# Performance work log

Hardware: AMD Instinct MI355X
Metric: run time of the kernel (lower is better)

The kernel has to match this reference:

```python
import jax, jax.numpy as jnp
import numpy as np

B = 8192
DV = 768   # visual_input_size
DT = 768   # text_input_size
E = 8      # num_experts
D = 1024   # expert_output_size
G = 2 * D  # gate_input_size
EPS = 1e-5


def setup_inputs() -> dict:
    key = jax.random.key(0)
    ks = jax.random.split(key, 14)
    s = lambda fan_in: 1.0 / np.sqrt(fan_in)
    return {
        "visual_features": jax.random.normal(ks[0], (B, DV), dtype=jnp.float32),
        "text_features": jax.random.normal(ks[1], (B, DT), dtype=jnp.float32),
        "vis_w": jax.random.uniform(ks[2], (DV, D), jnp.float32, -s(DV), s(DV)),
        "vis_b": jax.random.uniform(ks[3], (D,), jnp.float32, -s(DV), s(DV)),
        "txt_w": jax.random.uniform(ks[4], (DT, D), jnp.float32, -s(DT), s(DT)),
        "txt_b": jax.random.uniform(ks[5], (D,), jnp.float32, -s(DT), s(DT)),
        "gate_w": jax.random.uniform(ks[6], (G, E), jnp.float32, -s(G), s(G)),
        "gate_b": jax.random.uniform(ks[7], (E,), jnp.float32, -s(G), s(G)),
        "w1": jax.random.uniform(ks[8], (E, G, D), jnp.float32, -s(G), s(G)),
        "b1": jax.random.uniform(ks[9], (E, D), jnp.float32, -s(G), s(G)),
        "w2": jax.random.uniform(ks[10], (E, D, D), jnp.float32, -s(D), s(D)),
        "b2": jax.random.uniform(ks[11], (E, D), jnp.float32, -s(D), s(D)),
        "ln_g": jnp.ones((E, D), dtype=jnp.float32),
        "ln_b": jnp.zeros((E, D), dtype=jnp.float32),
    }


def reference(visual_features, text_features, vis_w, vis_b, txt_w, txt_b,
              gate_w, gate_b, w1, b1, w2, b2, ln_g, ln_b):
    # Projections + concat -> combined features [B, 2D]
    pv = visual_features @ vis_w + vis_b
    pt = text_features @ txt_w + txt_b
    combined = jnp.concatenate([pv, pt], axis=1)

    # Gate (dropout is identity at inference)
    gate_probs = jax.nn.softmax(combined @ gate_w + gate_b, axis=1)  # [B, E]

    # All experts as batched GEMMs: [B,G] x [E,G,D] -> [B,E,D]
    h = jnp.einsum('bg,egd->bed', combined, w1) + b1
    h = jax.nn.gelu(h, approximate=False)  # torch nn.GELU default = exact erf
    h = jnp.einsum('bed,edo->beo', h, w2) + b2

    # Per-expert LayerNorm over last dim
    mu = jnp.mean(h, axis=-1, keepdims=True)
    var = jnp.mean(jnp.square(h - mu), axis=-1, keepdims=True)
    h = (h - mu) * jax.lax.rsqrt(var + EPS) * ln_g + ln_b

    # Gated reduction over experts
    return jnp.einsum('bed,be->bd', h, gate_probs)
```

## Files before the change

### kernel.cpp

```cpp
#include <hip/hip_runtime.h>
#include <hip/hip_bf16.h>
#include <math.h>

#define BM 128
#define BN 128
#define BK 64

typedef __bf16 bf16x8_t __attribute__((ext_vector_type(8)));
typedef __bf16 bf16x4_t __attribute__((ext_vector_type(4)));
typedef float f32x16_t __attribute__((ext_vector_type(16)));

static __device__ __forceinline__ float bf2f(__bf16 b) {
    unsigned short s = __builtin_bit_cast(unsigned short, b);
    unsigned int u = ((unsigned int)s) << 16;
    return __builtin_bit_cast(float, u);
}
static __device__ __forceinline__ __bf16 f2bf(float f) {
    unsigned int u = __builtin_bit_cast(unsigned int, f);
    unsigned int r = (u + 0x7fffu + ((u >> 16) & 1u)) >> 16;
    return __builtin_bit_cast(__bf16, (unsigned short)r);
}
static __device__ __forceinline__ float gelu_fast(float x) {
    const float s = x * (0.7978845608f + 0.0356774081f * x * x);
    const float e = __expf(-2.0f * s);
    return x * __builtin_amdgcn_rcpf(1.0f + e);
}

#define GLDS16(gp, lp)                                                                   \
    __builtin_amdgcn_global_load_lds((const __attribute__((address_space(1))) void*)(gp), \
                                     (__attribute__((address_space(3))) void*)(lp), 16, 0, 0)

__global__ __launch_bounds__(256) void frag_cast(const float* __restrict__ in,
                                                 __bf16* __restrict__ out,
                                                 int K, int N,
                                                 size_t inStride, size_t outStride) {
    in += (size_t)blockIdx.z * inStride;
    out += (size_t)blockIdx.z * outStride;
    __shared__ float tile[64][65];
    const int k0 = blockIdx.x * 64, n0 = blockIdx.y * 64;
    const int tid = threadIdx.x;
    const int r = tid >> 4, c4 = (tid & 15) * 4;
#pragma unroll
    for (int p = 0; p < 4; ++p) {
        const float4 v = *(const float4*)&in[(size_t)(k0 + r + p * 16) * N + n0 + c4];
        tile[r + p * 16][c4 + 0] = v.x;
        tile[r + p * 16][c4 + 1] = v.y;
        tile[r + p * 16][c4 + 2] = v.z;
        tile[r + p * 16][c4 + 3] = v.w;
    }
    __syncthreads();
    const int c = tid >> 5, nn0 = (tid & 31) * 2;
#pragma unroll
    for (int t = 0; t < 2; ++t) {
        const int nn = nn0 + t;
        bf16x8_t v;
#pragma unroll
        for (int j = 0; j < 8; ++j) v[j] = f2bf(tile[c * 8 + j][nn]);
        *(bf16x8_t*)&out[((size_t)(k0 >> 3) + c) * N * 8 + (size_t)(n0 + nn) * 8] = v;
    }
}

__global__ __launch_bounds__(256) void cast2_kernel(const float* __restrict__ a,
                                                    const float* __restrict__ b,
                                                    __bf16* __restrict__ out, int n8each) {
    const int i = blockIdx.x * 256 + threadIdx.x;
    if (i < 2 * n8each) {
        const float* src = (i < n8each) ? a : b;
        const size_t idx = (i < n8each) ? (size_t)i : (size_t)(i - n8each);
        const float4* p = (const float4*)(src + idx * 8);
        const float4 x = p[0], y = p[1];
        bf16x8_t v;
        v[0] = f2bf(x.x); v[1] = f2bf(x.y); v[2] = f2bf(x.z); v[3] = f2bf(x.w);
        v[4] = f2bf(y.x); v[5] = f2bf(y.y); v[6] = f2bf(y.z); v[7] = f2bf(y.w);
        *(bf16x8_t*)(out + (size_t)i * 8) = v;
    }
}

__global__ __launch_bounds__(256) void cast_acat(const float* __restrict__ vis,
                                                 const float* __restrict__ txt,
                                                 __bf16* __restrict__ out, int total8) {
    const int i = blockIdx.x * 256 + threadIdx.x;
    if (i < total8) {
        const int r = i / 192;
        const int c8 = i - r * 192;
        const float* src = (c8 < 96) ? vis + (size_t)r * 768 + (size_t)c8 * 8
                                     : txt + (size_t)r * 768 + (size_t)(c8 - 96) * 8;
        const float4* p = (const float4*)src;
        const float4 x = p[0], y = p[1];
        bf16x8_t v;
        v[0] = f2bf(x.x); v[1] = f2bf(x.y); v[2] = f2bf(x.z); v[3] = f2bf(x.w);
        v[4] = f2bf(y.x); v[5] = f2bf(y.y); v[6] = f2bf(y.z); v[7] = f2bf(y.w);
        *(bf16x8_t*)(out + (size_t)i * 8) = v;
    }
}

template <int ACT, int PACK>
static __device__ __forceinline__ void gemm_core(const __bf16* __restrict__ A, int lda,
                                                 const __bf16* __restrict__ Bt, int Bn,
                                                 const float* __restrict__ bias,
                                                 __bf16* __restrict__ C, int ldc, int K,
                                                 int bm, int bn, __bf16* As) {
    const int tid = threadIdx.x;
    const int lane = tid & 63, wave = tid >> 6;
    const int wm = wave >> 1, wn = wave & 1;
    const int l = lane & 31, hi = lane >> 5;

    const int srow = tid >> 3;
    const int schunk = (tid & 7) ^ (srow & 7);
    const __bf16* ag = A + (size_t)(bm * BM + srow) * lda + schunk * 8;
    __bf16* asl = As + tid * 8;

    const int c0 = hi ^ (l & 7);
    const __bf16* base_a = As + (size_t)(wm * 64 + l) * BK;

    const size_t Bn8 = (size_t)Bn * 8;
    const __bf16* bbase = Bt + (size_t)hi * Bn8 + (size_t)(bn * BN + wn * 64 + l) * 8;

    f32x16_t acc[2][2] = {};

    const int nk = K / BK;
    for (int kt = 0; kt < nk; ++kt) {
        bf16x8_t bfr[4][2];
        const __bf16* bp = bbase + (size_t)(kt * 8) * Bn8;
#pragma unroll
        for (int s = 0; s < 4; ++s) {
            bfr[s][0] = *(const bf16x8_t*)(bp + (size_t)(2 * s) * Bn8);
            bfr[s][1] = *(const bf16x8_t*)(bp + (size_t)(2 * s) * Bn8 + 256);
        }
        GLDS16(ag, asl);
        GLDS16(ag + (size_t)32 * lda, asl + 2048);
        GLDS16(ag + (size_t)64 * lda, asl + 4096);
        GLDS16(ag + (size_t)96 * lda, asl + 6144);
        ag += BK;
        __syncthreads();
#pragma unroll
        for (int s = 0; s < 4; ++s) {
            const int co = (c0 ^ (2 * s)) * 8;
            const bf16x8_t a0 = *(const bf16x8_t*)(base_a + co);
            const bf16x8_t a1 = *(const bf16x8_t*)(base_a + 2048 + co);
            acc[0][0] = __builtin_amdgcn_mfma_f32_32x32x16_bf16(a0, bfr[s][0], acc[0][0], 0, 0, 0);
            acc[0][1] = __builtin_amdgcn_mfma_f32_32x32x16_bf16(a0, bfr[s][1], acc[0][1], 0, 0, 0);
            acc[1][0] = __builtin_amdgcn_mfma_f32_32x32x16_bf16(a1, bfr[s][0], acc[1][0], 0, 0, 0);
            acc[1][1] = __builtin_amdgcn_mfma_f32_32x32x16_bf16(a1, bfr[s][1], acc[1][1], 0, 0, 0);
        }
        __syncthreads();
    }

    const int colbase = bn * BN + wn * 64 + l;
    const int rowbase = bm * BM + wm * 64 + 4 * hi;
#pragma unroll
    for (int ni = 0; ni < 2; ++ni) {
        const int col = colbase + ni * 32;
        const float bv = PACK ? 0.0f : bias[col];
#pragma unroll
        for (int mi = 0; mi < 2; ++mi) {
#pragma unroll
            for (int v = 0; v < 16; ++v) {
                const int row = rowbase + mi * 32 + (v & 3) + 8 * (v >> 2);
                float x = acc[mi][ni][v] + bv;
                if (ACT == 1) x = gelu_fast(x);
                if (PACK) {
                    C[((size_t)(row >> 3)) * (size_t)ldc * 8 + (size_t)col * 8 + (row & 7)] = f2bf(x);
                } else {
                    C[(size_t)row * ldc + col] = f2bf(x);
                }
            }
        }
    }
}

template <int ACT>
__global__ __launch_bounds__(256) void gemm_bt(const __bf16* __restrict__ Ab, int lda, size_t strideAe,
                                               const __bf16* __restrict__ Bb, int Bn, size_t strideBe,
                                               const float* __restrict__ biasb, size_t strideBiasE,
                                               __bf16* __restrict__ Cb, int ldc, size_t strideCe,
                                               int K) {
    __shared__ __bf16 As[BM * BK];
    gemm_core<ACT, 0>(Ab + (size_t)blockIdx.z * strideAe, lda,
                      Bb + (size_t)blockIdx.z * strideBe, Bn,
                      biasb + (size_t)blockIdx.z * strideBiasE,
                      Cb + (size_t)blockIdx.z * strideCe, ldc, K,
                      blockIdx.x, blockIdx.y, As);
}

__global__ __launch_bounds__(256) void gemm_premul(const __bf16* __restrict__ wbf,
                                                   const __bf16* __restrict__ w1t,
                                                   __bf16* __restrict__ w1cat) {
    __shared__ __bf16 As[BM * BK];
    const int e = blockIdx.z & 7, hf = blockIdx.z >> 3;
    gemm_core<0, 1>(wbf + (size_t)hf * 768 * 1024, 1024,
                    w1t + (size_t)e * 2048 * 1024 + (size_t)hf * 128 * 1024 * 8, 1024,
                    nullptr,
                    w1cat + (size_t)e * 1536 * 1024 + (size_t)hf * 96 * 1024 * 8, 1024, 1024,
                    blockIdx.x, blockIdx.y, As);
}

__global__ __launch_bounds__(256) void bias1_kernel(const float* __restrict__ w1,
                                                    const float* __restrict__ vis_b,
                                                    const float* __restrict__ txt_b,
                                                    const float* __restrict__ b1,
                                                    float* __restrict__ b1t) {
    const int n = blockIdx.x * 256 + threadIdx.x;
    const int e = blockIdx.y;
    const int d0 = blockIdx.z * 512;
    float acc = (blockIdx.z == 0) ? b1[(size_t)e * 1024 + n] : 0.0f;
#pragma unroll 4
    for (int d = d0; d < d0 + 512; ++d) {
        const float bv = (d < 1024) ? vis_b[d] : txt_b[d - 1024];
        acc += bv * w1[((size_t)e * 2048 + d) * 1024 + n];
    }
    atomicAdd(&b1t[(size_t)e * 1024 + n], acc);
}

__global__ __launch_bounds__(256) void gcat_kernel(const float* __restrict__ vis_w,
                                                   const float* __restrict__ txt_w,
                                                   const float* __restrict__ vis_b,
                                                   const float* __restrict__ txt_b,
                                                   const float* __restrict__ gw,
                                                   const float* __restrict__ gb,
                                                   float* __restrict__ gcat) {
    const int v = blockIdx.x, tid = threadIdx.x;
    const int lane = tid & 63, wv = tid >> 6;
    float a[8] = {0, 0, 0, 0, 0, 0, 0, 0};
    if (v < 1536) {
        const float* wr = (v < 768) ? vis_w + (size_t)v * 1024 : txt_w + (size_t)(v - 768) * 1024;
        const int dbase = (v < 768) ? 0 : 1024;
        for (int d = tid; d < 1024; d += 256) {
            const float c = wr[d];
            const float4* g4 = (const float4*)(gw + (size_t)(dbase + d) * 8);
            const float4 x = g4[0], y = g4[1];
            a[0] += c * x.x; a[1] += c * x.y; a[2] += c * x.z; a[3] += c * x.w;
            a[4] += c * y.x; a[5] += c * y.y; a[6] += c * y.z; a[7] += c * y.w;
        }
    } else {
        for (int d = tid; d < 2048; d += 256) {
            const float c = (d < 1024) ? vis_b[d] : txt_b[d - 1024];
            const float4* g4 = (const float4*)(gw + (size_t)d * 8);
            const float4 x = g4[0], y = g4[1];
            a[0] += c * x.x; a[1] += c * x.y; a[2] += c * x.z; a[3] += c * x.w;
            a[4] += c * y.x; a[5] += c * y.y; a[6] += c * y.z; a[7] += c * y.w;
        }
    }
#pragma unroll
    for (int j = 0; j < 8; ++j)
        for (int off = 32; off; off >>= 1) a[j] += __shfl_down(a[j], off, 64);
    __shared__ float red[4][8];
    if (lane == 0) {
#pragma unroll
        for (int j = 0; j < 8; ++j) red[wv][j] = a[j];
    }
    __syncthreads();
    if (tid < 8) {
        float s = red[0][tid] + red[1][tid] + red[2][tid] + red[3][tid];
        if (v == 1536) s += gb[tid];
        gcat[(size_t)v * 8 + tid] = s;
    }
}

__global__ __launch_bounds__(256) void gate_kernel(const __bf16* __restrict__ acat,
                                                   const float* __restrict__ gcat,
                                                   float* __restrict__ gate) {
    const int b = blockIdx.x, tid = threadIdx.x;
    const int lane = tid & 63, wv = tid >> 6;
    const __bf16* row = acat + (size_t)b * 1536;
    float a[8] = {0, 0, 0, 0, 0, 0, 0, 0};
    for (int k = tid; k < 1536; k += 256) {
        const float c = bf2f(row[k]);
        const float4* g4 = (const float4*)(gcat + (size_t)k * 8);
        const float4 x = g4[0], y = g4[1];
        a[0] += c * x.x; a[1] += c * x.y; a[2] += c * x.z; a[3] += c * x.w;
        a[4] += c * y.x; a[5] += c * y.y; a[6] += c * y.z; a[7] += c * y.w;
    }
#pragma unroll
    for (int j = 0; j < 8; ++j)
        for (int off = 32; off; off >>= 1) a[j] += __shfl_down(a[j], off, 64);
    __shared__ float red[4][8];
    if (lane == 0) {
#pragma unroll
        for (int j = 0; j < 8; ++j) red[wv][j] = a[j];
    }
    __syncthreads();
    if (tid == 0) {
        const float* bg = gcat + 1536 * 8;
        float l[8];
        float m = -1e30f;
        for (int j = 0; j < 8; ++j) {
            l[j] = red[0][j] + red[1][j] + red[2][j] + red[3][j] + bg[j];
            m = fmaxf(m, l[j]);
        }
        float s = 0.f;
        for (int j = 0; j < 8; ++j) { l[j] = expf(l[j] - m); s += l[j]; }
        const float inv = 1.0f / s;
        for (int j = 0; j < 8; ++j) gate[(size_t)b * 8 + j] = l[j] * inv;
    }
}

__global__ __launch_bounds__(256) void ln_out_kernel(const __bf16* __restrict__ h2,
                                                     const float* __restrict__ gate,
                                                     const float* __restrict__ lng,
                                                     const float* __restrict__ lnb,
                                                     float* __restrict__ out,
                                                     int Eg, int g0, int accum) {
    const int b = blockIdx.x;
    const int tid = threadIdx.x;
    const int lane = tid & 63, wv = tid >> 6;
    const int d0 = tid * 4;
    __shared__ float sS[4], sSS[4];
    float* orow = out + (size_t)b * 1024 + d0;
    float o0, o1, o2, o3;
    if (accum) {
        const float4 p = *(const float4*)orow;
        o0 = p.x; o1 = p.y; o2 = p.z; o3 = p.w;
    } else {
        o0 = o1 = o2 = o3 = 0.f;
    }
    for (int e = 0; e < Eg; ++e) {
        const __bf16* hp = h2 + ((size_t)e * 8192 + b) * 1024 + d0;
        const bf16x4_t hv = *(const bf16x4_t*)hp;
        const float v0 = bf2f(hv[0]), v1 = bf2f(hv[1]), v2 = bf2f(hv[2]), v3 = bf2f(hv[3]);
        float s = v0 + v1 + v2 + v3;
        float ss = v0 * v0 + v1 * v1 + v2 * v2 + v3 * v3;
        for (int off = 32; off; off >>= 1) {
            s += __shfl_down(s, off, 64);
            ss += __shfl_down(ss, off, 64);
        }
        if (lane == 0) { sS[wv] = s; sSS[wv] = ss; }
        __syncthreads();
        const float S = sS[0] + sS[1] + sS[2] + sS[3];
        const float SS = sSS[0] + sSS[1] + sSS[2] + sSS[3];
        __syncthreads();
        const float mu = S * (1.0f / 1024.0f);
        const float var = SS * (1.0f / 1024.0f) - mu * mu;
        const float rstd = rsqrtf(var + 1e-5f);
        const float w = gate[(size_t)b * 8 + g0 + e];
        const float4 gg = *(const float4*)(lng + (size_t)(g0 + e) * 1024 + d0);
        const float4 bb = *(const float4*)(lnb + (size_t)(g0 + e) * 1024 + d0);
        o0 += w * ((v0 - mu) * rstd * gg.x + bb.x);
        o1 += w * ((v1 - mu) * rstd * gg.y + bb.y);
        o2 += w * ((v2 - mu) * rstd * gg.z + bb.z);
        o3 += w * ((v3 - mu) * rstd * gg.w + bb.w);
    }
    *(float4*)orow = make_float4(o0, o1, o2, o3);
}

extern "C" void kernel_launch(void* const* d_in, const int* in_sizes, int n_in,
                              void* d_out, int out_size, void* d_ws, size_t ws_size,
                              hipStream_t stream) {
    (void)in_sizes; (void)n_in; (void)out_size;
    const float* visual = (const float*)d_in[0];
    const float* text   = (const float*)d_in[1];
    const float* vis_w  = (const float*)d_in[2];
    const float* vis_b  = (const float*)d_in[3];
    const float* txt_w  = (const float*)d_in[4];
    const float* txt_b  = (const float*)d_in[5];
    const float* gate_w = (const float*)d_in[6];
    const float* gate_b = (const float*)d_in[7];
    const float* w1     = (const float*)d_in[8];
    const float* b1     = (const float*)d_in[9];
    const float* w2     = (const float*)d_in[10];
    const float* b2     = (const float*)d_in[11];
    const float* ln_g   = (const float*)d_in[12];
    const float* ln_b   = (const float*)d_in[13];
    float* out = (float*)d_out;

    const size_t B = 8192, DV = 768, D = 1024, G = 2048, E = 8, KC = 1536;

    char* ws = (char*)d_ws;
    size_t o = 0;
    auto alloc = [&](size_t bytes) { size_t r = o; o = (o + bytes + 255) & ~(size_t)255; return r; };
    const size_t off_wbf   = alloc(2 * DV * D * 2);
    const size_t off_w1cat = alloc(E * KC * D * 2);
    const size_t off_w2t   = alloc(E * D * D * 2);
    const size_t off_b1t   = alloc(E * D * 4);
    const size_t off_gcat  = alloc((KC * E + E) * 4);
    const size_t off_gate  = alloc(B * E * 4);
    const size_t off_acat  = alloc(B * KC * 2);
    const size_t fixedEnd = o;
    const size_t w1tBytes = E * G * D * 2;

    int Eg = 1;
    {
        const int cand[4] = {8, 4, 2, 1};
        for (int c = 0; c < 4; ++c) {
            size_t h2b = 2 * (size_t)cand[c] * B * D * 2;
            size_t dyn = h2b > w1tBytes ? h2b : w1tBytes;
            if (fixedEnd + dyn <= ws_size || cand[c] == 1) { Eg = cand[c]; break; }
        }
    }

    __bf16* wbf   = (__bf16*)(ws + off_wbf);
    __bf16* w1cat = (__bf16*)(ws + off_w1cat);
    __bf16* w2t   = (__bf16*)(ws + off_w2t);
    float*  b1t   = (float*)(ws + off_b1t);
    float*  gcat  = (float*)(ws + off_gcat);
    float*  gate  = (float*)(ws + off_gate);
    __bf16* acat  = (__bf16*)(ws + off_acat);
    __bf16* w1t   = (__bf16*)(ws + fixedEnd);
    __bf16* h1    = (__bf16*)(ws + fixedEnd);
    __bf16* h2    = h1 + (size_t)Eg * B * D;

    const int nw8 = (int)(DV * D / 8);
    cast2_kernel<<<(2 * nw8 + 255) / 256, 256, 0, stream>>>(vis_w, txt_w, wbf, nw8);
    const int na8 = (int)(B * KC / 8);
    cast_acat<<<(na8 + 255) / 256, 256, 0, stream>>>(visual, text, acat, na8);

    frag_cast<<<dim3(G / 64, D / 64, E), 256, 0, stream>>>(w1, w1t, (int)G, (int)D, G * D, G * D);
    frag_cast<<<dim3(D / 64, D / 64, E), 256, 0, stream>>>(w2, w2t, (int)D, (int)D, D * D, D * D);

    gemm_premul<<<dim3(768 / BM, D / BN, 16), 256, 0, stream>>>(wbf, w1t, w1cat);

    hipMemsetAsync(b1t, 0, E * D * 4, stream);
    bias1_kernel<<<dim3(4, 8, 4), 256, 0, stream>>>(w1, vis_b, txt_b, b1, b1t);
    gcat_kernel<<<1537, 256, 0, stream>>>(vis_w, txt_w, vis_b, txt_b, gate_w, gate_b, gcat);

    gate_kernel<<<(int)B, 256, 0, stream>>>(acat, gcat, gate);

    const int ng = 8 / Eg;
    for (int g = 0; g < ng; ++g) {
        const int g0 = g * Eg;
        gemm_bt<1><<<dim3(B / BM, D / BN, Eg), 256, 0, stream>>>(
            acat, (int)KC, 0, w1cat + (size_t)g0 * KC * D, (int)D, KC * D,
            b1t + (size_t)g0 * D, D, h1, (int)D, B * D, (int)KC);
        gemm_bt<0><<<dim3(B / BM, D / BN, Eg), 256, 0, stream>>>(
            h1, (int)D, B * D, w2t + (size_t)g0 * D * D, (int)D, D * D,
            b2 + (size_t)g0 * D, D, h2, (int)D, B * D, (int)D);
        ln_out_kernel<<<(int)B, 256, 0, stream>>>(h2, gate, ln_g, ln_b, out, Eg, g0, g > 0 ? 1 : 0);
    }
}
```

Baseline: 793.9 us.

## Use 256x256 tiles with double-buffered LDS for both GEMM operands

```diff
diff --git a/kernel.cpp b/kernel.cpp
--- a/kernel.cpp
+++ b/kernel.cpp
@@ -2,8 +2,8 @@
 #include <hip/hip_bf16.h>
 #include <math.h>
 
-#define BM 128
-#define BN 128
+#define BM 256
+#define BN 256
 #define BK 64
 
 typedef __bf16 bf16x8_t __attribute__((ext_vector_type(8)));
@@ -94,66 +94,107 @@
     }
 }
 
+#define MFMA32(a, b, c) __builtin_amdgcn_mfma_f32_32x32x16_bf16(a, b, c, 0, 0, 0)
+
 template <int ACT, int PACK>
 static __device__ __forceinline__ void gemm_core(const __bf16* __restrict__ A, int lda,
                                                  const __bf16* __restrict__ Bt, int Bn,
                                                  const float* __restrict__ bias,
                                                  __bf16* __restrict__ C, int ldc, int K,
-                                                 int bm, int bn, __bf16* As) {
+                                                 int bm, int bn,
+                                                 __bf16* As, __bf16* Bs) {
     const int tid = threadIdx.x;
     const int lane = tid & 63, wave = tid >> 6;
-    const int wm = wave >> 1, wn = wave & 1;
+    const int wm = wave >> 2, wn = wave & 3;
     const int l = lane & 31, hi = lane >> 5;
 
-    const int srow = tid >> 3;
-    const int schunk = (tid & 7) ^ (srow & 7);
-    const __bf16* ag = A + (size_t)(bm * BM + srow) * lda + schunk * 8;
-    __bf16* asl = As + tid * 8;
-
-    const int c0 = hi ^ (l & 7);
-    const __bf16* base_a = As + (size_t)(wm * 64 + l) * BK;
-
     const size_t Bn8 = (size_t)Bn * 8;
-    const __bf16* bbase = Bt + (size_t)hi * Bn8 + (size_t)(bn * BN + wn * 64 + l) * 8;
-
-    f32x16_t acc[2][2] = {};
+    const size_t bKt = Bn8 * 8;
+    const size_t BUFE = 8 * 256 * 8;
+
+    const __bf16* aSrc[4];
+    const __bf16* bSrc[4];
+    __bf16* aDst[4];
+    __bf16* bDst[4];
+#pragma unroll
+    for (int r = 0; r < 4; ++r) {
+        const int idx = r * 512 + tid;
+        const int ch = idx >> 8, rw = idx & 255;
+        aSrc[r] = A + (size_t)(bm * BM + rw) * lda + ch * 8;
+        bSrc[r] = Bt + (size_t)ch * Bn8 + (size_t)(bn * BN + rw) * 8;
+        aDst[r] = As + (size_t)idx * 8;
+        bDst[r] = Bs + (size_t)idx * 8;
+    }
+
+    const __bf16* aRd = As + ((size_t)hi * 256 + wm * 128 + l) * 8;
+    const __bf16* bRd = Bs + ((size_t)hi * 256 + wn * 64 + l) * 8;
+
+    f32x16_t acc[4][2] = {};
+
+#pragma unroll
+    for (int r = 0; r < 4; ++r) {
+        GLDS16(aSrc[r], aDst[r]);
+        GLDS16(bSrc[r], bDst[r]);
+    }
+    asm volatile("s_waitcnt vmcnt(0)");
+    __builtin_amdgcn_s_barrier();
+    __builtin_amdgcn_sched_barrier(0);
 
     const int nk = K / BK;
     for (int kt = 0; kt < nk; ++kt) {
-        bf16x8_t bfr[4][2];
-        const __bf16* bp = bbase + (size_t)(kt * 8) * Bn8;
+        const int cur = kt & 1;
+        const int nxt = cur ^ 1;
+        const int ktn = (kt + 1 < nk) ? kt + 1 : kt;
+        const __bf16* aR = aRd + (size_t)cur * BUFE;
+        const __bf16* bR = bRd + (size_t)cur * BUFE;
 #pragma unroll
         for (int s = 0; s < 4; ++s) {
-            bfr[s][0] = *(const bf16x8_t*)(bp + (size_t)(2 * s) * Bn8);
-            bfr[s][1] = *(const bf16x8_t*)(bp + (size_t)(2 * s) * Bn8 + 256);
-        }
-        GLDS16(ag, asl);
-        GLDS16(ag + (size_t)32 * lda, asl + 2048);
-        GLDS16(ag + (size_t)64 * lda, asl + 4096);
-        GLDS16(ag + (size_t)96 * lda, asl + 6144);
-        ag += BK;
-        __syncthreads();
-#pragma unroll
-        for (int s = 0; s < 4; ++s) {
-            const int co = (c0 ^ (2 * s)) * 8;
-            const bf16x8_t a0 = *(const bf16x8_t*)(base_a + co);
-            const bf16x8_t a1 = *(const bf16x8_t*)(base_a + 2048 + co);
-            acc[0][0] = __builtin_amdgcn_mfma_f32_32x32x16_bf16(a0, bfr[s][0], acc[0][0], 0, 0, 0);
-            acc[0][1] = __builtin_amdgcn_mfma_f32_32x32x16_bf16(a0, bfr[s][1], acc[0][1], 0, 0, 0);
-            acc[1][0] = __builtin_amdgcn_mfma_f32_32x32x16_bf16(a1, bfr[s][0], acc[1][0], 0, 0, 0);
-            acc[1][1] = __builtin_amdgcn_mfma_f32_32x32x16_bf16(a1, bfr[s][1], acc[1][1], 0, 0, 0);
-        }
-        __syncthreads();
+            const size_t co = (size_t)(2 * s) * 2048;
+            const bf16x8_t a0 = *(const bf16x8_t*)(aR + co);
+            const bf16x8_t a1 = *(const bf16x8_t*)(aR + co + 256);
+            const bf16x8_t a2 = *(const bf16x8_t*)(aR + co + 512);
+            const bf16x8_t a3 = *(const bf16x8_t*)(aR + co + 768);
+            const bf16x8_t b0 = *(const bf16x8_t*)(bR + co);
+            const bf16x8_t b1 = *(const bf16x8_t*)(bR + co + 256);
+            if (s == 0) {
+                GLDS16(aSrc[0] + (size_t)ktn * BK, aDst[0] + nxt * BUFE);
+                GLDS16(bSrc[0] + (size_t)ktn * bKt, bDst[0] + nxt * BUFE);
+                GLDS16(aSrc[1] + (size_t)ktn * BK, aDst[1] + nxt * BUFE);
+                GLDS16(bSrc[1] + (size_t)ktn * bKt, bDst[1] + nxt * BUFE);
+            } else if (s == 1) {
+                GLDS16(aSrc[2] + (size_t)ktn * BK, aDst[2] + nxt * BUFE);
+                GLDS16(bSrc[2] + (size_t)ktn * bKt, bDst[2] + nxt * BUFE);
+                GLDS16(aSrc[3] + (size_t)ktn * BK, aDst[3] + nxt * BUFE);
+                GLDS16(bSrc[3] + (size_t)ktn * bKt, bDst[3] + nxt * BUFE);
+            }
+            __builtin_amdgcn_sched_barrier(0);
+            __builtin_amdgcn_s_barrier();
+            __builtin_amdgcn_sched_barrier(0);
+            __builtin_amdgcn_s_setprio(1);
+            acc[0][0] = MFMA32(a0, b0, acc[0][0]);
+            acc[0][1] = MFMA32(a0, b1, acc[0][1]);
+            acc[1][0] = MFMA32(a1, b0, acc[1][0]);
+            acc[1][1] = MFMA32(a1, b1, acc[1][1]);
+            acc[2][0] = MFMA32(a2, b0, acc[2][0]);
+            acc[2][1] = MFMA32(a2, b1, acc[2][1]);
+            acc[3][0] = MFMA32(a3, b0, acc[3][0]);
+            acc[3][1] = MFMA32(a3, b1, acc[3][1]);
+            __builtin_amdgcn_s_setprio(0);
+            if (s == 3) asm volatile("s_waitcnt vmcnt(0)");
+            __builtin_amdgcn_sched_barrier(0);
+            __builtin_amdgcn_s_barrier();
+            __builtin_amdgcn_sched_barrier(0);
+        }
     }
 
     const int colbase = bn * BN + wn * 64 + l;
-    const int rowbase = bm * BM + wm * 64 + 4 * hi;
+    const int rowbase = bm * BM + wm * 128 + 4 * hi;
 #pragma unroll
     for (int ni = 0; ni < 2; ++ni) {
         const int col = colbase + ni * 32;
         const float bv = PACK ? 0.0f : bias[col];
 #pragma unroll
-        for (int mi = 0; mi < 2; ++mi) {
+        for (int mi = 0; mi < 4; ++mi) {
 #pragma unroll
             for (int v = 0; v < 16; ++v) {
                 const int row = rowbase + mi * 32 + (v & 3) + 8 * (v >> 2);
@@ -170,29 +211,31 @@
 }
 
 template <int ACT>
-__global__ __launch_bounds__(256) void gemm_bt(const __bf16* __restrict__ Ab, int lda, size_t strideAe,
-                                               const __bf16* __restrict__ Bb, int Bn, size_t strideBe,
-                                               const float* __restrict__ biasb, size_t strideBiasE,
-                                               __bf16* __restrict__ Cb, int ldc, size_t strideCe,
-                                               int K) {
-    __shared__ __bf16 As[BM * BK];
+__global__ __launch_bounds__(512, 2) void gemm_bt(const __bf16* __restrict__ Ab, int lda, size_t strideAe,
+                                                  const __bf16* __restrict__ Bb, int Bn, size_t strideBe,
+                                                  const float* __restrict__ biasb, size_t strideBiasE,
+                                                  __bf16* __restrict__ Cb, int ldc, size_t strideCe,
+                                                  int K) {
+    __shared__ __bf16 As[2 * 8 * 256 * 8];
+    __shared__ __bf16 Bs[2 * 8 * 256 * 8];
     gemm_core<ACT, 0>(Ab + (size_t)blockIdx.z * strideAe, lda,
                       Bb + (size_t)blockIdx.z * strideBe, Bn,
                       biasb + (size_t)blockIdx.z * strideBiasE,
                       Cb + (size_t)blockIdx.z * strideCe, ldc, K,
-                      blockIdx.x, blockIdx.y, As);
-}
-
-__global__ __launch_bounds__(256) void gemm_premul(const __bf16* __restrict__ wbf,
-                                                   const __bf16* __restrict__ w1t,
-                                                   __bf16* __restrict__ w1cat) {
-    __shared__ __bf16 As[BM * BK];
+                      blockIdx.x, blockIdx.y, As, Bs);
+}
+
+__global__ __launch_bounds__(512, 2) void gemm_premul(const __bf16* __restrict__ wbf,
+                                                      const __bf16* __restrict__ w1t,
+                                                      __bf16* __restrict__ w1cat) {
+    __shared__ __bf16 As[2 * 8 * 256 * 8];
+    __shared__ __bf16 Bs[2 * 8 * 256 * 8];
     const int e = blockIdx.z & 7, hf = blockIdx.z >> 3;
     gemm_core<0, 1>(wbf + (size_t)hf * 768 * 1024, 1024,
                     w1t + (size_t)e * 2048 * 1024 + (size_t)hf * 128 * 1024 * 8, 1024,
                     nullptr,
                     w1cat + (size_t)e * 1536 * 1024 + (size_t)hf * 96 * 1024 * 8, 1024, 1024,
-                    blockIdx.x, blockIdx.y, As);
+                    blockIdx.x, blockIdx.y, As, Bs);
 }
 
 __global__ __launch_bounds__(256) void bias1_kernel(const float* __restrict__ w1,
@@ -407,7 +450,7 @@
     frag_cast<<<dim3(G / 64, D / 64, E), 256, 0, stream>>>(w1, w1t, (int)G, (int)D, G * D, G * D);
     frag_cast<<<dim3(D / 64, D / 64, E), 256, 0, stream>>>(w2, w2t, (int)D, (int)D, D * D, D * D);
 
-    gemm_premul<<<dim3(768 / BM, D / BN, 16), 256, 0, stream>>>(wbf, w1t, w1cat);
+    gemm_premul<<<dim3(768 / BM, D / BN, 16), 512, 0, stream>>>(wbf, w1t, w1cat);
 
     hipMemsetAsync(b1t, 0, E * D * 4, stream);
     bias1_kernel<<<dim3(4, 8, 4), 256, 0, stream>>>(w1, vis_b, txt_b, b1, b1t);
@@ -418,10 +461,10 @@
     const int ng = 8 / Eg;
     for (int g = 0; g < ng; ++g) {
         const int g0 = g * Eg;
-        gemm_bt<1><<<dim3(B / BM, D / BN, Eg), 256, 0, stream>>>(
+        gemm_bt<1><<<dim3(B / BM, D / BN, Eg), 512, 0, stream>>>(
             acat, (int)KC, 0, w1cat + (size_t)g0 * KC * D, (int)D, KC * D,
             b1t + (size_t)g0 * D, D, h1, (int)D, B * D, (int)KC);
-        gemm_bt<0><<<dim3(B / BM, D / BN, Eg), 256, 0, stream>>>(
+        gemm_bt<0><<<dim3(B / BM, D / BN, Eg), 512, 0, stream>>>(
             h1, (int)D, B * D, w2t + (size_t)g0 * D * D, (int)D, D * D,
             b2 + (size_t)g0 * D, D, h2, (int)D, B * D, (int)D);
         ln_out_kernel<<<(int)B, 256, 0, stream>>>(h2, gate, ln_g, ln_b, out, Eg, g0, g > 0 ? 1 : 0);
```

Result: slower. 893.4 us (+12.5%).

## Store GEMM A operands in 128-row k-chunk tiled layout for contiguous loads

Applied to the files above, without the earlier changes.

```diff
diff --git a/kernel.cpp b/kernel.cpp
--- a/kernel.cpp
+++ b/kernel.cpp
@@ -65,14 +65,18 @@
                                                     __bf16* __restrict__ out, int n8each) {
     const int i = blockIdx.x * 256 + threadIdx.x;
     if (i < 2 * n8each) {
-        const float* src = (i < n8each) ? a : b;
-        const size_t idx = (i < n8each) ? (size_t)i : (size_t)(i - n8each);
-        const float4* p = (const float4*)(src + idx * 8);
+        const int m = (i < n8each) ? 0 : 1;
+        const int ii = i - m * n8each;
+        const float* src = (m ? b : a) + (size_t)ii * 8;
+        const int r = ii >> 7, c8 = ii & 127;
+        const size_t dst = (size_t)m * 786432 + (size_t)(r >> 7) * 131072 +
+                           (size_t)c8 * 1024 + (size_t)(r & 127) * 8;
+        const float4* p = (const float4*)src;
         const float4 x = p[0], y = p[1];
         bf16x8_t v;
         v[0] = f2bf(x.x); v[1] = f2bf(x.y); v[2] = f2bf(x.z); v[3] = f2bf(x.w);
         v[4] = f2bf(y.x); v[5] = f2bf(y.y); v[6] = f2bf(y.z); v[7] = f2bf(y.w);
-        *(bf16x8_t*)(out + (size_t)i * 8) = v;
+        *(bf16x8_t*)(out + dst) = v;
     }
 }
 
@@ -90,58 +94,59 @@
         bf16x8_t v;
         v[0] = f2bf(x.x); v[1] = f2bf(x.y); v[2] = f2bf(x.z); v[3] = f2bf(x.w);
         v[4] = f2bf(y.x); v[5] = f2bf(y.y); v[6] = f2bf(y.z); v[7] = f2bf(y.w);
-        *(bf16x8_t*)(out + (size_t)i * 8) = v;
-    }
-}
+        const size_t dst = (size_t)(r >> 7) * 196608 + (size_t)c8 * 1024 +
+                           (size_t)(r & 127) * 8;
+        *(bf16x8_t*)(out + dst) = v;
+    }
+}
+
+#define MFMA32(a, b, c) __builtin_amdgcn_mfma_f32_32x32x16_bf16(a, b, c, 0, 0, 0)
 
 template <int ACT, int PACK>
-static __device__ __forceinline__ void gemm_core(const __bf16* __restrict__ A, int lda,
+static __device__ __forceinline__ void gemm_core(const __bf16* __restrict__ A, int K,
                                                  const __bf16* __restrict__ Bt, int Bn,
                                                  const float* __restrict__ bias,
-                                                 __bf16* __restrict__ C, int ldc, int K,
+                                                 __bf16* __restrict__ C, int ldc,
                                                  int bm, int bn, __bf16* As) {
     const int tid = threadIdx.x;
     const int lane = tid & 63, wave = tid >> 6;
     const int wm = wave >> 1, wn = wave & 1;
     const int l = lane & 31, hi = lane >> 5;
 
-    const int srow = tid >> 3;
-    const int schunk = (tid & 7) ^ (srow & 7);
-    const __bf16* ag = A + (size_t)(bm * BM + srow) * lda + schunk * 8;
+    const __bf16* ag = A + (size_t)bm * K * 128 + (size_t)tid * 8;
     __bf16* asl = As + tid * 8;
 
-    const int c0 = hi ^ (l & 7);
-    const __bf16* base_a = As + (size_t)(wm * 64 + l) * BK;
+    const __bf16* base_a = As + hi * 1024 + (wm * 64 + l) * 8;
 
     const size_t Bn8 = (size_t)Bn * 8;
     const __bf16* bbase = Bt + (size_t)hi * Bn8 + (size_t)(bn * BN + wn * 64 + l) * 8;
+    const size_t bAdv = 8 * Bn8;
 
     f32x16_t acc[2][2] = {};
 
     const int nk = K / BK;
     for (int kt = 0; kt < nk; ++kt) {
         bf16x8_t bfr[4][2];
-        const __bf16* bp = bbase + (size_t)(kt * 8) * Bn8;
 #pragma unroll
         for (int s = 0; s < 4; ++s) {
-            bfr[s][0] = *(const bf16x8_t*)(bp + (size_t)(2 * s) * Bn8);
-            bfr[s][1] = *(const bf16x8_t*)(bp + (size_t)(2 * s) * Bn8 + 256);
+            bfr[s][0] = *(const bf16x8_t*)(bbase + (size_t)(2 * s) * Bn8);
+            bfr[s][1] = *(const bf16x8_t*)(bbase + (size_t)(2 * s) * Bn8 + 256);
         }
         GLDS16(ag, asl);
-        GLDS16(ag + (size_t)32 * lda, asl + 2048);
-        GLDS16(ag + (size_t)64 * lda, asl + 4096);
-        GLDS16(ag + (size_t)96 * lda, asl + 6144);
-        ag += BK;
+        GLDS16(ag + 2048, asl + 2048);
+        GLDS16(ag + 4096, asl + 4096);
+        GLDS16(ag + 6144, asl + 6144);
+        ag += 8192;
+        bbase += bAdv;
         __syncthreads();
 #pragma unroll
         for (int s = 0; s < 4; ++s) {
-            const int co = (c0 ^ (2 * s)) * 8;
-            const bf16x8_t a0 = *(const bf16x8_t*)(base_a + co);
-            const bf16x8_t a1 = *(const bf16x8_t*)(base_a + 2048 + co);
-            acc[0][0] = __builtin_amdgcn_mfma_f32_32x32x16_bf16(a0, bfr[s][0], acc[0][0], 0, 0, 0);
-            acc[0][1] = __builtin_amdgcn_mfma_f32_32x32x16_bf16(a0, bfr[s][1], acc[0][1], 0, 0, 0);
-            acc[1][0] = __builtin_amdgcn_mfma_f32_32x32x16_bf16(a1, bfr[s][0], acc[1][0], 0, 0, 0);
-            acc[1][1] = __builtin_amdgcn_mfma_f32_32x32x16_bf16(a1, bfr[s][1], acc[1][1], 0, 0, 0);
+            const bf16x8_t a0 = *(const bf16x8_t*)(base_a + s * 2048);
+            const bf16x8_t a1 = *(const bf16x8_t*)(base_a + s * 2048 + 256);
+            acc[0][0] = MFMA32(a0, bfr[s][0], acc[0][0]);
+            acc[0][1] = MFMA32(a0, bfr[s][1], acc[0][1]);
+            acc[1][0] = MFMA32(a1, bfr[s][0], acc[1][0]);
+            acc[1][1] = MFMA32(a1, bfr[s][1], acc[1][1]);
         }
         __syncthreads();
     }
@@ -151,7 +156,7 @@
 #pragma unroll
     for (int ni = 0; ni < 2; ++ni) {
         const int col = colbase + ni * 32;
-        const float bv = PACK ? 0.0f : bias[col];
+        const float bv = (PACK == 1) ? 0.0f : bias[col];
 #pragma unroll
         for (int mi = 0; mi < 2; ++mi) {
 #pragma unroll
@@ -159,8 +164,11 @@
                 const int row = rowbase + mi * 32 + (v & 3) + 8 * (v >> 2);
                 float x = acc[mi][ni][v] + bv;
                 if (ACT == 1) x = gelu_fast(x);
-                if (PACK) {
+                if (PACK == 1) {
                     C[((size_t)(row >> 3)) * (size_t)ldc * 8 + (size_t)col * 8 + (row & 7)] = f2bf(x);
+                } else if (PACK == 2) {
+                    C[(size_t)(row >> 7) * (size_t)ldc * 128 + (size_t)(col >> 3) * 1024 +
+                      (size_t)(row & 127) * 8 + (col & 7)] = f2bf(x);
                 } else {
                     C[(size_t)row * ldc + col] = f2bf(x);
                 }
@@ -169,18 +177,17 @@
     }
 }
 
-template <int ACT>
-__global__ __launch_bounds__(256) void gemm_bt(const __bf16* __restrict__ Ab, int lda, size_t strideAe,
+template <int ACT, int PACK>
+__global__ __launch_bounds__(256) void gemm_bt(const __bf16* __restrict__ Ab, int K, size_t strideAe,
                                                const __bf16* __restrict__ Bb, int Bn, size_t strideBe,
                                                const float* __restrict__ biasb, size_t strideBiasE,
-                                               __bf16* __restrict__ Cb, int ldc, size_t strideCe,
-                                               int K) {
+                                               __bf16* __restrict__ Cb, int ldc, size_t strideCe) {
     __shared__ __bf16 As[BM * BK];
-    gemm_core<ACT, 0>(Ab + (size_t)blockIdx.z * strideAe, lda,
-                      Bb + (size_t)blockIdx.z * strideBe, Bn,
-                      biasb + (size_t)blockIdx.z * strideBiasE,
-                      Cb + (size_t)blockIdx.z * strideCe, ldc, K,
-                      blockIdx.x, blockIdx.y, As);
+    gemm_core<ACT, PACK>(Ab + (size_t)blockIdx.z * strideAe, K,
+                         Bb + (size_t)blockIdx.z * strideBe, Bn,
+                         biasb + (size_t)blockIdx.z * strideBiasE,
+                         Cb + (size_t)blockIdx.z * strideCe, ldc,
+                         blockIdx.x, blockIdx.y, As);
 }
 
 __global__ __launch_bounds__(256) void gemm_premul(const __bf16* __restrict__ wbf,
@@ -188,10 +195,10 @@
                                                    __bf16* __restrict__ w1cat) {
     __shared__ __bf16 As[BM * BK];
     const int e = blockIdx.z & 7, hf = blockIdx.z >> 3;
-    gemm_core<0, 1>(wbf + (size_t)hf * 768 * 1024, 1024,
+    gemm_core<0, 1>(wbf + (size_t)hf * 786432, 1024,
                     w1t + (size_t)e * 2048 * 1024 + (size_t)hf * 128 * 1024 * 8, 1024,
                     nullptr,
-                    w1cat + (size_t)e * 1536 * 1024 + (size_t)hf * 96 * 1024 * 8, 1024, 1024,
+                    w1cat + (size_t)e * 1536 * 1024 + (size_t)hf * 96 * 1024 * 8, 1024,
                     blockIdx.x, blockIdx.y, As);
 }
 
@@ -262,14 +269,18 @@
                                                    float* __restrict__ gate) {
     const int b = blockIdx.x, tid = threadIdx.x;
     const int lane = tid & 63, wv = tid >> 6;
-    const __bf16* row = acat + (size_t)b * 1536;
+    const __bf16* base = acat + (size_t)(b >> 7) * 196608 + (size_t)(b & 127) * 8;
     float a[8] = {0, 0, 0, 0, 0, 0, 0, 0};
-    for (int k = tid; k < 1536; k += 256) {
-        const float c = bf2f(row[k]);
-        const float4* g4 = (const float4*)(gcat + (size_t)k * 8);
-        const float4 x = g4[0], y = g4[1];
-        a[0] += c * x.x; a[1] += c * x.y; a[2] += c * x.z; a[3] += c * x.w;
-        a[4] += c * y.x; a[5] += c * y.y; a[6] += c * y.z; a[7] += c * y.w;
+    if (tid < 192) {
+        const bf16x8_t av = *(const bf16x8_t*)(base + (size_t)tid * 1024);
+#pragma unroll
+        for (int jj = 0; jj < 8; ++jj) {
+            const float c = bf2f(av[jj]);
+            const float4* g4 = (const float4*)(gcat + (size_t)(tid * 8 + jj) * 8);
+            const float4 x = g4[0], y = g4[1];
+            a[0] += c * x.x; a[1] += c * x.y; a[2] += c * x.z; a[3] += c * x.w;
+            a[4] += c * y.x; a[5] += c * y.y; a[6] += c * y.z; a[7] += c * y.w;
+        }
     }
 #pragma unroll
     for (int j = 0; j < 8; ++j)
@@ -418,12 +429,12 @@
     const int ng = 8 / Eg;
     for (int g = 0; g < ng; ++g) {
         const int g0 = g * Eg;
-        gemm_bt<1><<<dim3(B / BM, D / BN, Eg), 256, 0, stream>>>(
+        gemm_bt<1, 2><<<dim3(B / BM, D / BN, Eg), 256, 0, stream>>>(
             acat, (int)KC, 0, w1cat + (size_t)g0 * KC * D, (int)D, KC * D,
-            b1t + (size_t)g0 * D, D, h1, (int)D, B * D, (int)KC);
-        gemm_bt<0><<<dim3(B / BM, D / BN, Eg), 256, 0, stream>>>(
+            b1t + (size_t)g0 * D, D, h1, (int)D, B * D);
+        gemm_bt<0, 0><<<dim3(B / BM, D / BN, Eg), 256, 0, stream>>>(
             h1, (int)D, B * D, w2t + (size_t)g0 * D * D, (int)D, D * D,
-            b2 + (size_t)g0 * D, D, h2, (int)D, B * D, (int)D);
+            b2 + (size_t)g0 * D, D, h2, (int)D, B * D);
         ln_out_kernel<<<(int)B, 256, 0, stream>>>(h2, gate, ln_g, ln_b, out, Eg, g0, g > 0 ? 1 : 0);
     }
 }
```

Result: slower. 825.7 us (+4.0%).
